# Optimization experiments

Hardware: AMD Instinct MI355X
Metric: run time of the kernel (lower is better)

## Reference

```python
import jax, jax.numpy as jnp
import numpy as np
from jax import lax

H = 16  # hidden size

def lstm_dir(x_tbd, Wih, Whh, bih, bhh):
    # x_tbd: [T, B, D] -> outputs [T, B, H], final h [B, H]
    T, B, _ = x_tbd.shape
    xg = jnp.einsum('tbd,gd->tbg', x_tbd, Wih) + bih + bhh  # [T, B, 4H]
    def step(carry, xt):
        h, c = carry
        g = xt + h @ Whh.T
        i, f, gg, o = jnp.split(g, 4, axis=-1)  # PyTorch gate order i,f,g,o
        i = jax.nn.sigmoid(i); f = jax.nn.sigmoid(f)
        gg = jnp.tanh(gg); o = jax.nn.sigmoid(o)
        c = f * c + i * gg
        h = o * jnp.tanh(c)
        return (h, c), h
    init = (jnp.zeros((B, H), x_tbd.dtype), jnp.zeros((B, H), x_tbd.dtype))
    (hT, cT), hs = lax.scan(step, init, xg)
    return hs, hT

def bi_layer(x_tbd, pf, pb):
    hs_f, hT_f = lstm_dir(x_tbd, *pf)
    hs_b_rev, hT_b = lstm_dir(x_tbd[::-1], *pb)
    out = jnp.concatenate([hs_f, hs_b_rev[::-1]], axis=-1)  # [T, B, 2H]
    return out, hT_f, hT_b


def setup_inputs() -> dict:
    key = jax.random.key(0)
    ks = iter(jax.random.split(key, 32))
    B, T = 4096, 512
    d = {"x": jax.random.normal(next(ks), (B, T), jnp.float32)}
    def w(shape):
        return jax.random.normal(next(ks), shape, jnp.float32) * 0.2
    # layer 0 (input dim 1), forward / backward directions
    for s in ('f', 'b'):
        d[f'Wih0{s}'] = w((4 * H, 1)); d[f'Whh0{s}'] = w((4 * H, H))
        d[f'bih0{s}'] = jnp.zeros((4 * H,), jnp.float32)
        d[f'bhh0{s}'] = jnp.zeros((4 * H,), jnp.float32)
    # layer 1 (input dim 2H = 32)
    for s in ('f', 'b'):
        d[f'Wih1{s}'] = w((4 * H, 2 * H)); d[f'Whh1{s}'] = w((4 * H, H))
        d[f'bih1{s}'] = jnp.zeros((4 * H,), jnp.float32)
        d[f'bhh1{s}'] = jnp.zeros((4 * H,), jnp.float32)
    # MLP head: Linear(32,25), Linear(25,20)
    d['W1'] = w((25, 2 * H)); d['b1'] = jnp.zeros((25,), jnp.float32)
    d['W2'] = w((20, 25)); d['b2'] = jnp.zeros((20,), jnp.float32)
    return d


def reference(x, Wih0f, Whh0f, bih0f, bhh0f, Wih0b, Whh0b, bih0b, bhh0b,
              Wih1f, Whh1f, bih1f, bhh1f, Wih1b, Whh1b, bih1b, bhh1b,
              W1, b1, W2, b2):
    # x: [B, T] -> unsqueeze(2) -> [B, T, 1]; scan over time, so transpose to [T, B, 1]
    x_tbd = x.T[:, :, None]
    o0, _, _ = bi_layer(x_tbd, (Wih0f, Whh0f, bih0f, bhh0f), (Wih0b, Whh0b, bih0b, bhh0b))
    # dropout=0.1 between layers is inactive in eval mode (reference = eval)
    _, hT_f, hT_b = bi_layer(o0, (Wih1f, Whh1f, bih1f, bhh1f), (Wih1b, Whh1b, bih1b, bhh1b))
    # torch: cat((h[-1], h[-2]), 1) = (last-layer backward, last-layer forward)
    feat = jnp.concatenate([hT_b, hT_f], axis=1)  # [B, 32]
    z = jax.nn.elu(feat)
    z = jax.nn.elu(z @ W1.T + b1)
    z = jax.nn.elu(z @ W2.T + b2)
    return z  # [B, 20]
```

## Files before the change

kernel.cpp:

```cpp
#include <hip/hip_runtime.h>
#include <stdint.h>

#define TT 512
#define BB 4096
#define NT8 512
#define LOG2E 1.4426950408889634f

typedef _Float16 half8_t __attribute__((ext_vector_type(8)));
typedef __fp16 fp16x2_t __attribute__((ext_vector_type(2)));
typedef float f32x4 __attribute__((ext_vector_type(4)));
typedef float f32x2 __attribute__((ext_vector_type(2)));

union FragU { uint4 u4; half8_t h8; };
union PkU { fp16x2_t h2; unsigned int u; };

__device__ __forceinline__ float rcp_(float x){ return __builtin_amdgcn_rcpf(x); }
__device__ __forceinline__ float exp2_(float x){ return __builtin_amdgcn_exp2f(x); }
__device__ __forceinline__ float elu_(float x){ return x > 0.0f ? x : (exp2_(x * LOG2E) - 1.0f); }
__device__ __forceinline__ int mini_(int a, int b){ return a < b ? a : b; }
__device__ __forceinline__ float maskhi_(float x){ return __uint_as_float(__float_as_uint(x) & 0xFFFFE000u); }
__device__ __forceinline__ unsigned int pkrtz_(float a, float b){
    PkU p; p.h2 = __builtin_amdgcn_cvt_pkrtz(a, b); return p.u;
}

__device__ __forceinline__ f32x4 MFMA(half8_t a, half8_t b, f32x4 c) {
    return __builtin_amdgcn_mfma_f32_16x16x32_f16(a, b, c, 0, 0, 0);
}

__device__ __forceinline__ f32x4 ld4_(const float* p){ return *(const f32x4*)p; }

__device__ __forceinline__ half8_t packA8s(const float* s, float sc) {
    half8_t h;
#pragma unroll
    for (int k = 0; k < 8; ++k) h[k] = (_Float16)(s[k] * sc);
    return h;
}

__device__ __forceinline__ void cell2p_(f32x2 gi, f32x2 gf, f32x2 gg, f32x2 go,
                                        f32x2& c, f32x2& h) {
    f32x2 ei, ef, eg, eo;
    ei[0] = exp2_(-gi[0]); ei[1] = exp2_(-gi[1]);
    ef[0] = exp2_(-gf[0]); ef[1] = exp2_(-gf[1]);
    eg[0] = exp2_(-gg[0]); eg[1] = exp2_(-gg[1]);
    eo[0] = exp2_(-go[0]); eo[1] = exp2_(-go[1]);
    const f32x2 one = {1.0f, 1.0f};
    f32x2 ai = one + ei, af = one + ef, ag = one + eg, ao = one + eo;
    f32x2 pif = ai * af, pgo = ag * ao;
    f32x2 P = pif * pgo;
    f32x2 R; R[0] = rcp_(P[0]); R[1] = rcp_(P[1]);
    f32x2 I = R * (af * pgo);
    f32x2 F = R * (ai * pgo);
    f32x2 Gt = R * (pif * ao);
    f32x2 O = R * (pif * ag);
    f32x2 G = Gt + Gt - one;
    c = F * c + I * G;
    f32x2 ct = c * (-2.0f * LOG2E);
    f32x2 et; et[0] = exp2_(ct[0]); et[1] = exp2_(ct[1]);
    f32x2 den = one + et;
    f32x2 Rt; Rt[0] = rcp_(den[0]); Rt[1] = rcp_(den[1]);
    f32x2 T = Rt + Rt - one;
    h = O * T;
}


struct PA {
    const float *x;
    const float *WihF, *WhhF, *bihF, *bhhF;
    const float *WihB, *WhhB, *bihB, *bhhB;
    char* ws;
};

__global__ __launch_bounds__(256) void phaseA_k(PA p) {
    __shared__ uint4 lds4[4 * 48];
    const int tid = threadIdx.x;
    const int lane = tid & 63;
    const int wv   = tid >> 6;
    char* lds = (char*)lds4 + wv * 768;
    const int q = lane >> 4, b = lane & 15, c = b & 7;
    const bool hi8 = b >= 8;
    const int chain = blockIdx.x * 4 + wv;
    const int tile = chain >> 1, dir = chain & 1;

    const float* Wih = dir ? p.WihB : p.WihF;
    const float* Whh = dir ? p.WhhB : p.WhhF;
    const float* bih = dir ? p.bihB : p.bihF;
    const float* bhh = dir ? p.bhhB : p.bhhF;

    const float SC0 = LOG2E, SC1 = LOG2E, SC2 = 2.0f*LOG2E, SC3 = LOG2E;

    half8_t whh0 = packA8s(Whh + (     b)*16 + 8*(q&1), SC0);
    half8_t whh1 = packA8s(Whh + (16 + b)*16 + 8*(q&1), SC1);
    half8_t whh2 = packA8s(Whh + (32 + b)*16 + 8*(q&1), SC2);
    half8_t whh3 = packA8s(Whh + (48 + b)*16 + 8*(q&1), SC3);

    f32x4 bias0 = (ld4_(bih +      4*q) + ld4_(bhh +      4*q)) * SC0;
    f32x4 bias1 = (ld4_(bih + 16 + 4*q) + ld4_(bhh + 16 + 4*q)) * SC1;
    f32x4 bias2 = (ld4_(bih + 32 + 4*q) + ld4_(bhh + 32 + 4*q)) * SC2;
    f32x4 bias3 = (ld4_(bih + 48 + 4*q) + ld4_(bhh + 48 + 4*q)) * SC3;

    f32x4 wihx0 = ld4_(Wih +      4*q) * SC0;
    f32x4 wihx1 = ld4_(Wih + 16 + 4*q) * SC1;
    f32x4 wihx2 = ld4_(Wih + 32 + 4*q) * SC2;
    f32x4 wihx3 = ld4_(Wih + 48 + 4*q) * SC3;

    const int uu  = 4*q + (hi8 ? 2 : 0);
    const int rdo = c*80 + q*16;
    const int wro = c*80 + uu*2;

    { unsigned int* z = (unsigned int*)lds;
      for (int k = lane; k < 160; k += 64) z[k] = 0u; }
    __builtin_amdgcn_wave_barrier();

    f32x2 cc = {0.f, 0.f};

    const char* xbase = (const char*)p.x + (size_t)tile*8*TT*4;
    const int   xoff  = c*TT*4;
    char*       wsbase = p.ws + (size_t)tile*TT*512;
    const int   woff  = c*64 + dir*32 + uu*2;

    auto xld = [&](int u)->float {
        int s = mini_(u, TT-1);
        int t = dir ? (TT-1-s) : s;
        return *(const float*)(xbase + (size_t)t*4 + xoff);
    };

    auto step = [&](float xv, int t) {
        FragU hf; hf.u4 = *(const uint4*)(lds + rdo);
        f32x4 a0 = bias0 + wihx0 * xv;
        f32x4 a1 = bias1 + wihx1 * xv;
        f32x4 a2 = bias2 + wihx2 * xv;
        f32x4 a3 = bias3 + wihx3 * xv;
        a0 = MFMA(whh0, hf.h8, a0);
        a1 = MFMA(whh1, hf.h8, a1);
        a2 = MFMA(whh2, hf.h8, a2);
        a3 = MFMA(whh3, hf.h8, a3);
        f32x2 gi, gf, gg, go;
        gi[0] = hi8 ? a0[2] : a0[0]; gi[1] = hi8 ? a0[3] : a0[1];
        gf[0] = hi8 ? a1[2] : a1[0]; gf[1] = hi8 ? a1[3] : a1[1];
        gg[0] = hi8 ? a2[2] : a2[0]; gg[1] = hi8 ? a2[3] : a2[1];
        go[0] = hi8 ? a3[2] : a3[0]; go[1] = hi8 ? a3[3] : a3[1];
        f32x2 hh2;
        cell2p_(gi, gf, gg, go, cc, hh2);
        float m0 = maskhi_(hh2[0]), m1 = maskhi_(hh2[1]);
        unsigned int hh = pkrtz_(m0, m1), hl = pkrtz_(hh2[0] - m0, hh2[1] - m1);
        *(unsigned int*)(lds + wro) = hh;
        *(unsigned int*)(lds + wro + 32) = hl;
        *(unsigned int*)(wsbase + (size_t)t*512 + woff) = hh;
        __builtin_amdgcn_wave_barrier();
    };

    float xv0 = xld(0), xv1 = xld(1), xv2 = xld(2), xv3 = xld(3);
    for (int s = 0; s < TT; s += 4) {
        const int t0 = dir ? (TT-1-s) : s;
        const int d  = dir ? -1 : 1;
        step(xv0, t0      ); xv0 = xld(s+4);
        step(xv1, t0 + d  ); xv1 = xld(s+5);
        step(xv2, t0 + 2*d); xv2 = xld(s+6);
        step(xv3, t0 + 3*d); xv3 = xld(s+7);
    }
}

struct PB {
    const float *WihF, *WhhF, *bihF, *bhhF;
    const float *WihB, *WhhB, *bihB, *bhhB;
    const char* ws;
    float* hT;
};

__global__ __launch_bounds__(256) void phaseB_k(PB p) {
    __shared__ uint4 lds4[4 * 48];
    const int tid = threadIdx.x;
    const int lane = tid & 63;
    const int wv   = tid >> 6;
    char* lds = (char*)lds4 + wv * 768;
    const int q = lane >> 4, b = lane & 15, c = b & 7;
    const bool hi8 = b >= 8;
    const int chain = blockIdx.x * 4 + wv;
    const int tile = chain >> 1, dir = chain & 1;

    const float* Wih = dir ? p.WihB : p.WihF;
    const float* Whh = dir ? p.WhhB : p.WhhF;
    const float* bih = dir ? p.bihB : p.bihF;
    const float* bhh = dir ? p.bhhB : p.bhhF;

    const float SC0 = LOG2E, SC1 = LOG2E, SC2 = 2.0f*LOG2E, SC3 = LOG2E;

    half8_t wih0 = packA8s(Wih + (     b)*32 + 8*q, SC0);
    half8_t wih1 = packA8s(Wih + (16 + b)*32 + 8*q, SC1);
    half8_t wih2 = packA8s(Wih + (32 + b)*32 + 8*q, SC2);
    half8_t wih3 = packA8s(Wih + (48 + b)*32 + 8*q, SC3);

    half8_t whh0 = packA8s(Whh + (     b)*16 + 8*(q&1), SC0);
    half8_t whh1 = packA8s(Whh + (16 + b)*16 + 8*(q&1), SC1);
    half8_t whh2 = packA8s(Whh + (32 + b)*16 + 8*(q&1), SC2);
    half8_t whh3 = packA8s(Whh + (48 + b)*16 + 8*(q&1), SC3);

    f32x4 bias0 = (ld4_(bih +      4*q) + ld4_(bhh +      4*q)) * SC0;
    f32x4 bias1 = (ld4_(bih + 16 + 4*q) + ld4_(bhh + 16 + 4*q)) * SC1;
    f32x4 bias2 = (ld4_(bih + 32 + 4*q) + ld4_(bhh + 32 + 4*q)) * SC2;
    f32x4 bias3 = (ld4_(bih + 48 + 4*q) + ld4_(bhh + 48 + 4*q)) * SC3;

    const int uu  = 4*q + (hi8 ? 2 : 0);
    const int rdo = c*80 + q*16;
    const int wro = c*80 + uu*2;

    { unsigned int* z = (unsigned int*)lds;
      for (int k = lane; k < 160; k += 64) z[k] = 0u; }
    __builtin_amdgcn_wave_barrier();

    f32x2 cc = {0.f, 0.f};
    f32x2 hv = {0.f, 0.f};

    const char* wsbase = p.ws + (size_t)tile*TT*512;
    const int   xoff   = c*64 + q*16;

    auto xld = [&](int u)->uint4 {
        int s = mini_(u, TT-1);
        int t = dir ? (TT-1-s) : s;
        return *(const uint4*)(wsbase + (size_t)t*512 + xoff);
    };

    auto step = [&](uint4 xin) {
        FragU xf; xf.u4 = xin;
        FragU hf; hf.u4 = *(const uint4*)(lds + rdo);
        f32x4 a0 = MFMA(wih0, xf.h8, bias0);
        f32x4 a1 = MFMA(wih1, xf.h8, bias1);
        f32x4 a2 = MFMA(wih2, xf.h8, bias2);
        f32x4 a3 = MFMA(wih3, xf.h8, bias3);
        a0 = MFMA(whh0, hf.h8, a0);
        a1 = MFMA(whh1, hf.h8, a1);
        a2 = MFMA(whh2, hf.h8, a2);
        a3 = MFMA(whh3, hf.h8, a3);
        f32x2 gi, gf, gg, go;
        gi[0] = hi8 ? a0[2] : a0[0]; gi[1] = hi8 ? a0[3] : a0[1];
        gf[0] = hi8 ? a1[2] : a1[0]; gf[1] = hi8 ? a1[3] : a1[1];
        gg[0] = hi8 ? a2[2] : a2[0]; gg[1] = hi8 ? a2[3] : a2[1];
        go[0] = hi8 ? a3[2] : a3[0]; go[1] = hi8 ? a3[3] : a3[1];
        cell2p_(gi, gf, gg, go, cc, hv);
        float m0 = maskhi_(hv[0]), m1 = maskhi_(hv[1]);
        unsigned int hh = pkrtz_(m0, m1), hl = pkrtz_(hv[0] - m0, hv[1] - m1);
        *(unsigned int*)(lds + wro) = hh;
        *(unsigned int*)(lds + wro + 32) = hl;
        __builtin_amdgcn_wave_barrier();
    };

    uint4 xb0 = xld(0), xb1 = xld(1), xb2 = xld(2), xb3 = xld(3);
    for (int s = 0; s < TT; s += 4) {
        step(xb0); xb0 = xld(s+4);
        step(xb1); xb1 = xld(s+5);
        step(xb2); xb2 = xld(s+6);
        step(xb3); xb3 = xld(s+7);
    }

    float* hp = p.hT + ((size_t)(dir*NT8 + tile)*8 + c)*16 + uu;
    float2 ho; ho.x = hv[0]; ho.y = hv[1];
    *(float2*)hp = ho;
}

struct PC {
    const float* hT;
    const float *W1, *b1, *W2, *b2;
    float* out;
};

__global__ __launch_bounds__(64) void head_k(PC p) {
    const int B = blockIdx.x * 64 + threadIdx.x;
    const int tile = B >> 3, c = B & 7;
    const float* hf = p.hT + ((size_t)(         tile)*8 + c)*16;
    const float* hb = p.hT + ((size_t)(NT8 + tile)*8 + c)*16;

    float z0[32];
#pragma unroll
    for (int k = 0; k < 16; ++k) z0[k] = elu_(hb[k]);
#pragma unroll
    for (int k = 0; k < 16; ++k) z0[16+k] = elu_(hf[k]);

    float z1[25];
#pragma unroll
    for (int o = 0; o < 25; ++o) {
        float a = p.b1[o];
#pragma unroll
        for (int k = 0; k < 32; ++k) a = fmaf(p.W1[o*32 + k], z0[k], a);
        z1[o] = elu_(a);
    }
#pragma unroll
    for (int o = 0; o < 20; ++o) {
        float a = p.b2[o];
#pragma unroll
        for (int k = 0; k < 25; ++k) a = fmaf(p.W2[o*25 + k], z1[k], a);
        p.out[(size_t)B*20 + o] = elu_(a);
    }
}

extern "C" void kernel_launch(void* const* d_in, const int* in_sizes, int n_in,
                              void* d_out, int out_size, void* d_ws, size_t ws_size,
                              hipStream_t stream) {
    (void)in_sizes; (void)n_in; (void)out_size;

    const size_t frag_bytes = (size_t)NT8 * TT * 512;
    const size_t hT_bytes   = (size_t)2 * NT8 * 8 * 16 * sizeof(float);
    size_t hT_off = (ws_size >= frag_bytes + hT_bytes) ? frag_bytes
                                                       : (ws_size - hT_bytes);
    char* ws = (char*)d_ws;
    float* hT = (float*)(ws + hT_off);

    PA pa;
    pa.x = (const float*)d_in[0];
    pa.WihF = (const float*)d_in[1];  pa.WhhF = (const float*)d_in[2];
    pa.bihF = (const float*)d_in[3];  pa.bhhF = (const float*)d_in[4];
    pa.WihB = (const float*)d_in[5];  pa.WhhB = (const float*)d_in[6];
    pa.bihB = (const float*)d_in[7];  pa.bhhB = (const float*)d_in[8];
    pa.ws = ws;
    hipLaunchKernelGGL(phaseA_k, dim3(256), dim3(256), 0, stream, pa);

    PB pb;
    pb.WihF = (const float*)d_in[9];   pb.WhhF = (const float*)d_in[10];
    pb.bihF = (const float*)d_in[11];  pb.bhhF = (const float*)d_in[12];
    pb.WihB = (const float*)d_in[13];  pb.WhhB = (const float*)d_in[14];
    pb.bihB = (const float*)d_in[15];  pb.bhhB = (const float*)d_in[16];
    pb.ws = ws; pb.hT = hT;
    hipLaunchKernelGGL(phaseB_k, dim3(256), dim3(256), 0, stream, pb);

    PC pc;
    pc.hT = hT;
    pc.W1 = (const float*)d_in[17]; pc.b1 = (const float*)d_in[18];
    pc.W2 = (const float*)d_in[19]; pc.b2 = (const float*)d_in[20];
    pc.out = (float*)d_out;
    hipLaunchKernelGGL(head_k, dim3(BB/64), dim3(64), 0, stream, pc);
}
```

Baseline: 291.8 us.

## Pass hidden state by lane shuffles instead of LDS and fold x into MFMA

The recurrent hidden state no longer goes through an LDS round trip with a wave barrier between steps. Each lane now holds a single packed fp16 pair, and the MFMA B fragment is built from cross-lane shuffles. Phase A also folds the scalar input x into the same MFMA, splitting it into hi/lo fp16 parts in the unused K slots, which replaces the per-step vector FMAs. The h hi/lo split is dropped in favour of a single round-to-nearest fp16, so the recurrent path loses some precision in exchange for fewer conversions and stores.

```diff
diff --git a/kernel.cpp b/kernel.cpp
--- a/kernel.cpp
+++ b/kernel.cpp
@@ -22,6 +22,9 @@
 __device__ __forceinline__ unsigned int pkrtz_(float a, float b){
     PkU p; p.h2 = __builtin_amdgcn_cvt_pkrtz(a, b); return p.u;
 }
+__device__ __forceinline__ unsigned int pkrne_(float a, float b){
+    PkU p; p.h2[0] = (__fp16)a; p.h2[1] = (__fp16)b; return p.u;
+}
 
 __device__ __forceinline__ f32x4 MFMA(half8_t a, half8_t b, f32x4 c) {
     return __builtin_amdgcn_mfma_f32_16x16x32_f16(a, b, c, 0, 0, 0);
@@ -33,6 +36,12 @@
     half8_t h;
 #pragma unroll
     for (int k = 0; k < 8; ++k) h[k] = (_Float16)(s[k] * sc);
+    return h;
+}
+__device__ __forceinline__ half8_t zero8_() {
+    half8_t h;
+#pragma unroll
+    for (int k = 0; k < 8; ++k) h[k] = (_Float16)0.0f;
     return h;
 }
 
@@ -71,11 +80,9 @@
 };
 
 __global__ __launch_bounds__(256) void phaseA_k(PA p) {
-    __shared__ uint4 lds4[4 * 48];
     const int tid = threadIdx.x;
     const int lane = tid & 63;
     const int wv   = tid >> 6;
-    char* lds = (char*)lds4 + wv * 768;
     const int q = lane >> 4, b = lane & 15, c = b & 7;
     const bool hi8 = b >= 8;
     const int chain = blockIdx.x * 4 + wv;
@@ -86,31 +93,35 @@
     const float* bih = dir ? p.bihB : p.bihF;
     const float* bhh = dir ? p.bhhB : p.bhhF;
 
-    const float SC0 = LOG2E, SC1 = LOG2E, SC2 = 2.0f*LOG2E, SC3 = LOG2E;
-
-    half8_t whh0 = packA8s(Whh + (     b)*16 + 8*(q&1), SC0);
-    half8_t whh1 = packA8s(Whh + (16 + b)*16 + 8*(q&1), SC1);
-    half8_t whh2 = packA8s(Whh + (32 + b)*16 + 8*(q&1), SC2);
-    half8_t whh3 = packA8s(Whh + (48 + b)*16 + 8*(q&1), SC3);
-
-    f32x4 bias0 = (ld4_(bih +      4*q) + ld4_(bhh +      4*q)) * SC0;
-    f32x4 bias1 = (ld4_(bih + 16 + 4*q) + ld4_(bhh + 16 + 4*q)) * SC1;
-    f32x4 bias2 = (ld4_(bih + 32 + 4*q) + ld4_(bhh + 32 + 4*q)) * SC2;
-    f32x4 bias3 = (ld4_(bih + 48 + 4*q) + ld4_(bhh + 48 + 4*q)) * SC3;
-
-    f32x4 wihx0 = ld4_(Wih +      4*q) * SC0;
-    f32x4 wihx1 = ld4_(Wih + 16 + 4*q) * SC1;
-    f32x4 wihx2 = ld4_(Wih + 32 + 4*q) * SC2;
-    f32x4 wihx3 = ld4_(Wih + 48 + 4*q) * SC3;
-
-    const int uu  = 4*q + (hi8 ? 2 : 0);
-    const int rdo = c*80 + q*16;
-    const int wro = c*80 + uu*2;
-
-    { unsigned int* z = (unsigned int*)lds;
-      for (int k = lane; k < 160; k += 64) z[k] = 0u; }
-    __builtin_amdgcn_wave_barrier();
-
+    auto mkA = [&](int m, float sc)->half8_t {
+        if (q < 2) return packA8s(Whh + (16*m + b)*16 + 8*q, sc);
+        half8_t h = zero8_();
+        if (q == 2) {
+            float w = Wih[16*m + b] * sc;
+            h[0] = (_Float16)w;
+            h[1] = (_Float16)w;
+        }
+        return h;
+    };
+    half8_t A0 = mkA(0, LOG2E);
+    half8_t A1 = mkA(1, LOG2E);
+    half8_t A2 = mkA(2, 2.0f*LOG2E);
+    half8_t A3 = mkA(3, LOG2E);
+
+    f32x4 bias0 = (ld4_(bih +      4*q) + ld4_(bhh +      4*q)) * LOG2E;
+    f32x4 bias1 = (ld4_(bih + 16 + 4*q) + ld4_(bhh + 16 + 4*q)) * LOG2E;
+    f32x4 bias2 = (ld4_(bih + 32 + 4*q) + ld4_(bhh + 32 + 4*q)) * (2.0f*LOG2E);
+    f32x4 bias3 = (ld4_(bih + 48 + 4*q) + ld4_(bhh + 48 + 4*q)) * LOG2E;
+
+    const int uu = 4*q + (hi8 ? 2 : 0);
+    const int sa0 = 32*(q&1) + c;
+    const int sa1 = sa0 + 8;
+    const int sa2 = sa0 + 16;
+    const int sa3 = sa0 + 24;
+    const bool qlt2 = q < 2;
+    const bool q2   = q == 2;
+
+    unsigned int hh = 0u;
     f32x2 cc = {0.f, 0.f};
 
     const char* xbase = (const char*)p.x + (size_t)tile*8*TT*4;
@@ -118,35 +129,37 @@
     char*       wsbase = p.ws + (size_t)tile*TT*512;
     const int   woff  = c*64 + dir*32 + uu*2;
 
-    auto xld = [&](int u)->float {
-        int s = mini_(u, TT-1);
+    auto xld = [&](int s_)->float {
+        int s = mini_(s_, TT-1);
         int t = dir ? (TT-1-s) : s;
         return *(const float*)(xbase + (size_t)t*4 + xoff);
     };
 
     auto step = [&](float xv, int t) {
-        FragU hf; hf.u4 = *(const uint4*)(lds + rdo);
-        f32x4 a0 = bias0 + wihx0 * xv;
-        f32x4 a1 = bias1 + wihx1 * xv;
-        f32x4 a2 = bias2 + wihx2 * xv;
-        f32x4 a3 = bias3 + wihx3 * xv;
-        a0 = MFMA(whh0, hf.h8, a0);
-        a1 = MFMA(whh1, hf.h8, a1);
-        a2 = MFMA(whh2, hf.h8, a2);
-        a3 = MFMA(whh3, hf.h8, a3);
+        float mh = maskhi_(xv);
+        unsigned int xp = pkrtz_(mh, xv - mh);
+        unsigned int s0 = (unsigned int)__shfl((int)hh, sa0);
+        unsigned int s1 = (unsigned int)__shfl((int)hh, sa1);
+        unsigned int s2 = (unsigned int)__shfl((int)hh, sa2);
+        unsigned int s3 = (unsigned int)__shfl((int)hh, sa3);
+        FragU hf;
+        hf.u4.x = qlt2 ? s0 : (q2 ? xp : 0u);
+        hf.u4.y = qlt2 ? s1 : 0u;
+        hf.u4.z = qlt2 ? s2 : 0u;
+        hf.u4.w = qlt2 ? s3 : 0u;
+        f32x4 r0 = MFMA(A0, hf.h8, bias0);
+        f32x4 r1 = MFMA(A1, hf.h8, bias1);
+        f32x4 r2 = MFMA(A2, hf.h8, bias2);
+        f32x4 r3 = MFMA(A3, hf.h8, bias3);
         f32x2 gi, gf, gg, go;
-        gi[0] = hi8 ? a0[2] : a0[0]; gi[1] = hi8 ? a0[3] : a0[1];
-        gf[0] = hi8 ? a1[2] : a1[0]; gf[1] = hi8 ? a1[3] : a1[1];
-        gg[0] = hi8 ? a2[2] : a2[0]; gg[1] = hi8 ? a2[3] : a2[1];
-        go[0] = hi8 ? a3[2] : a3[0]; go[1] = hi8 ? a3[3] : a3[1];
-        f32x2 hh2;
-        cell2p_(gi, gf, gg, go, cc, hh2);
-        float m0 = maskhi_(hh2[0]), m1 = maskhi_(hh2[1]);
-        unsigned int hh = pkrtz_(m0, m1), hl = pkrtz_(hh2[0] - m0, hh2[1] - m1);
-        *(unsigned int*)(lds + wro) = hh;
-        *(unsigned int*)(lds + wro + 32) = hl;
+        gi[0] = hi8 ? r0[2] : r0[0]; gi[1] = hi8 ? r0[3] : r0[1];
+        gf[0] = hi8 ? r1[2] : r1[0]; gf[1] = hi8 ? r1[3] : r1[1];
+        gg[0] = hi8 ? r2[2] : r2[0]; gg[1] = hi8 ? r2[3] : r2[1];
+        go[0] = hi8 ? r3[2] : r3[0]; go[1] = hi8 ? r3[3] : r3[1];
+        f32x2 hv;
+        cell2p_(gi, gf, gg, go, cc, hv);
+        hh = pkrne_(hv[0], hv[1]);
         *(unsigned int*)(wsbase + (size_t)t*512 + woff) = hh;
-        __builtin_amdgcn_wave_barrier();
     };
 
     float xv0 = xld(0), xv1 = xld(1), xv2 = xld(2), xv3 = xld(3);
@@ -168,11 +181,9 @@
 };
 
 __global__ __launch_bounds__(256) void phaseB_k(PB p) {
-    __shared__ uint4 lds4[4 * 48];
     const int tid = threadIdx.x;
     const int lane = tid & 63;
     const int wv   = tid >> 6;
-    char* lds = (char*)lds4 + wv * 768;
     const int q = lane >> 4, b = lane & 15, c = b & 7;
     const bool hi8 = b >= 8;
     const int chain = blockIdx.x * 4 + wv;
@@ -185,63 +196,67 @@
 
     const float SC0 = LOG2E, SC1 = LOG2E, SC2 = 2.0f*LOG2E, SC3 = LOG2E;
 
-    half8_t wih0 = packA8s(Wih + (     b)*32 + 8*q, SC0);
-    half8_t wih1 = packA8s(Wih + (16 + b)*32 + 8*q, SC1);
-    half8_t wih2 = packA8s(Wih + (32 + b)*32 + 8*q, SC2);
-    half8_t wih3 = packA8s(Wih + (48 + b)*32 + 8*q, SC3);
-
-    half8_t whh0 = packA8s(Whh + (     b)*16 + 8*(q&1), SC0);
-    half8_t whh1 = packA8s(Whh + (16 + b)*16 + 8*(q&1), SC1);
-    half8_t whh2 = packA8s(Whh + (32 + b)*16 + 8*(q&1), SC2);
-    half8_t whh3 = packA8s(Whh + (48 + b)*16 + 8*(q&1), SC3);
+    half8_t wi0 = packA8s(Wih + (     b)*32 + 8*q, SC0);
+    half8_t wi1 = packA8s(Wih + (16 + b)*32 + 8*q, SC1);
+    half8_t wi2 = packA8s(Wih + (32 + b)*32 + 8*q, SC2);
+    half8_t wi3 = packA8s(Wih + (48 + b)*32 + 8*q, SC3);
+
+    half8_t wh0 = (q < 2) ? packA8s(Whh + (     b)*16 + 8*q, SC0) : zero8_();
+    half8_t wh1 = (q < 2) ? packA8s(Whh + (16 + b)*16 + 8*q, SC1) : zero8_();
+    half8_t wh2 = (q < 2) ? packA8s(Whh + (32 + b)*16 + 8*q, SC2) : zero8_();
+    half8_t wh3 = (q < 2) ? packA8s(Whh + (48 + b)*16 + 8*q, SC3) : zero8_();
 
     f32x4 bias0 = (ld4_(bih +      4*q) + ld4_(bhh +      4*q)) * SC0;
     f32x4 bias1 = (ld4_(bih + 16 + 4*q) + ld4_(bhh + 16 + 4*q)) * SC1;
     f32x4 bias2 = (ld4_(bih + 32 + 4*q) + ld4_(bhh + 32 + 4*q)) * SC2;
     f32x4 bias3 = (ld4_(bih + 48 + 4*q) + ld4_(bhh + 48 + 4*q)) * SC3;
 
-    const int uu  = 4*q + (hi8 ? 2 : 0);
-    const int rdo = c*80 + q*16;
-    const int wro = c*80 + uu*2;
-
-    { unsigned int* z = (unsigned int*)lds;
-      for (int k = lane; k < 160; k += 64) z[k] = 0u; }
-    __builtin_amdgcn_wave_barrier();
-
+    const int uu = 4*q + (hi8 ? 2 : 0);
+    const int sa0 = 32*(q&1) + c;
+    const int sa1 = sa0 + 8;
+    const int sa2 = sa0 + 16;
+    const int sa3 = sa0 + 24;
+    const bool qlt2 = q < 2;
+
+    unsigned int hh = 0u;
     f32x2 cc = {0.f, 0.f};
     f32x2 hv = {0.f, 0.f};
 
     const char* wsbase = p.ws + (size_t)tile*TT*512;
     const int   xoff   = c*64 + q*16;
 
-    auto xld = [&](int u)->uint4 {
-        int s = mini_(u, TT-1);
+    auto xld = [&](int s_)->uint4 {
+        int s = mini_(s_, TT-1);
         int t = dir ? (TT-1-s) : s;
         return *(const uint4*)(wsbase + (size_t)t*512 + xoff);
     };
 
     auto step = [&](uint4 xin) {
         FragU xf; xf.u4 = xin;
-        FragU hf; hf.u4 = *(const uint4*)(lds + rdo);
-        f32x4 a0 = MFMA(wih0, xf.h8, bias0);
-        f32x4 a1 = MFMA(wih1, xf.h8, bias1);
-        f32x4 a2 = MFMA(wih2, xf.h8, bias2);
-        f32x4 a3 = MFMA(wih3, xf.h8, bias3);
-        a0 = MFMA(whh0, hf.h8, a0);
-        a1 = MFMA(whh1, hf.h8, a1);
-        a2 = MFMA(whh2, hf.h8, a2);
-        a3 = MFMA(whh3, hf.h8, a3);
+        unsigned int s0 = (unsigned int)__shfl((int)hh, sa0);
+        unsigned int s1 = (unsigned int)__shfl((int)hh, sa1);
+        unsigned int s2 = (unsigned int)__shfl((int)hh, sa2);
+        unsigned int s3 = (unsigned int)__shfl((int)hh, sa3);
+        FragU hf;
+        hf.u4.x = qlt2 ? s0 : 0u;
+        hf.u4.y = qlt2 ? s1 : 0u;
+        hf.u4.z = qlt2 ? s2 : 0u;
+        hf.u4.w = qlt2 ? s3 : 0u;
+        f32x4 r0 = MFMA(wi0, xf.h8, bias0);
+        f32x4 r1 = MFMA(wi1, xf.h8, bias1);
+        f32x4 r2 = MFMA(wi2, xf.h8, bias2);
+        f32x4 r3 = MFMA(wi3, xf.h8, bias3);
+        r0 = MFMA(wh0, hf.h8, r0);
+        r1 = MFMA(wh1, hf.h8, r1);
+        r2 = MFMA(wh2, hf.h8, r2);
+        r3 = MFMA(wh3, hf.h8, r3);
         f32x2 gi, gf, gg, go;
-        gi[0] = hi8 ? a0[2] : a0[0]; gi[1] = hi8 ? a0[3] : a0[1];
-        gf[0] = hi8 ? a1[2] : a1[0]; gf[1] = hi8 ? a1[3] : a1[1];
-        gg[0] = hi8 ? a2[2] : a2[0]; gg[1] = hi8 ? a2[3] : a2[1];
-        go[0] = hi8 ? a3[2] : a3[0]; go[1] = hi8 ? a3[3] : a3[1];
+        gi[0] = hi8 ? r0[2] : r0[0]; gi[1] = hi8 ? r0[3] : r0[1];
+        gf[0] = hi8 ? r1[2] : r1[0]; gf[1] = hi8 ? r1[3] : r1[1];
+        gg[0] = hi8 ? r2[2] : r2[0]; gg[1] = hi8 ? r2[3] : r2[1];
+        go[0] = hi8 ? r3[2] : r3[0]; go[1] = hi8 ? r3[3] : r3[1];
         cell2p_(gi, gf, gg, go, cc, hv);
-        float m0 = maskhi_(hv[0]), m1 = maskhi_(hv[1]);
-        unsigned int hh = pkrtz_(m0, m1), hl = pkrtz_(hv[0] - m0, hv[1] - m1);
-        *(unsigned int*)(lds + wro) = hh;
-        *(unsigned int*)(lds + wro + 32) = hl;
-        __builtin_amdgcn_wave_barrier();
+        hh = pkrne_(hv[0], hv[1]);
     };
 
     uint4 xb0 = xld(0), xb1 = xld(1), xb2 = xld(2), xb3 = xld(3);
@@ -252,7 +267,8 @@
         step(xb3); xb3 = xld(s+7);
     }
 
-    float* hp = p.hT + ((size_t)(dir*NT8 + tile)*8 + c)*16 + uu;
+    const int batch = tile*8 + c;
+    float* hp = p.hT + ((size_t)(dir ? BB : 0) + batch)*16 + uu;
     float2 ho; ho.x = hv[0]; ho.y = hv[1];
     *(float2*)hp = ho;
 }
@@ -265,9 +281,8 @@
 
 __global__ __launch_bounds__(64) void head_k(PC p) {
     const int B = blockIdx.x * 64 + threadIdx.x;
-    const int tile = B >> 3, c = B & 7;
-    const float* hf = p.hT + ((size_t)(         tile)*8 + c)*16;
-    const float* hb = p.hT + ((size_t)(NT8 + tile)*8 + c)*16;
+    const float* hf = p.hT + (size_t)B*16;
+    const float* hb = p.hT + ((size_t)BB + B)*16;
 
     float z0[32];
 #pragma unroll
@@ -298,7 +313,7 @@
     (void)in_sizes; (void)n_in; (void)out_size;
 
     const size_t frag_bytes = (size_t)NT8 * TT * 512;
-    const size_t hT_bytes   = (size_t)2 * NT8 * 8 * 16 * sizeof(float);
+    const size_t hT_bytes   = (size_t)2 * BB * 16 * sizeof(float);
     size_t hT_off = (ws_size >= frag_bytes + hT_bytes) ? frag_bytes
                                                        : (ws_size - hT_bytes);
     char* ws = (char*)d_ws;
```

Result: slower. 306.3 us (+5.0%).
